# Kernel optimization log

Measured on AMD Instinct MI355X. Metric: run time of the kernel, lower is better.

## Reference

```python
import jax, jax.numpy as jnp
import numpy as np

N_NODES = 50000


def gcn_conv(x, src, dst, W, b, n_nodes):
    """PyG GCNConv: self-loops + symmetric normalization D^-1/2 (A+I) D^-1/2 X W + b."""
    loop = jnp.arange(n_nodes, dtype=src.dtype)
    s = jnp.concatenate([src, loop])
    d = jnp.concatenate([dst, loop])
    deg = jax.ops.segment_sum(jnp.ones_like(d, dtype=x.dtype), d, num_segments=n_nodes)
    dinv = jnp.where(deg > 0, jax.lax.rsqrt(deg), 0.0)
    norm = dinv[s] * dinv[d]  # (E+N,)
    h = x @ W  # (N, out)
    msg = h[s] * norm[:, None]
    return jax.ops.segment_sum(msg, d, num_segments=n_nodes) + b


def setup_inputs() -> dict:
    key = jax.random.key(0)
    ks = jax.random.split(key, 16)
    N, S, D = N_NODES, 20, 128
    E = 1_600_000
    PH, PO, GH, GO = 64, 128, 128, 32

    def lin(k, fan_in, fan_out):
        bound = 1.0 / np.sqrt(fan_in)
        kw, kb = jax.random.split(k)
        W = jax.random.uniform(kw, (fan_in, fan_out), jnp.float32, -bound, bound)
        b = jax.random.uniform(kb, (fan_out,), jnp.float32, -bound, bound)
        return W, b

    W_embed, b_embed = lin(ks[0], D, PH)
    W_attn, b_attn = lin(ks[1], PH, 1)
    W_out, b_out = lin(ks[2], PH, PO)
    W1, b1 = lin(ks[3], PO, GH)
    W2, b2 = lin(ks[4], GH, GO)
    Wm1, bm1 = lin(ks[5], GO, 64)
    Wm2, bm2 = lin(ks[6], 64, 1)

    return {
        "set_features": jax.random.normal(ks[7], (N, S, D), jnp.float32),
        "set_mask": jnp.ones((N, S), jnp.int32),
        "edge_index": jax.random.randint(ks[8], (2, E), 0, N, jnp.int32),
        "query_idx": jax.random.randint(ks[9], (4096,), 0, N, jnp.int32),
        "W_embed": W_embed, "b_embed": b_embed,
        "W_attn": W_attn, "b_attn": b_attn,
        "W_out": W_out, "b_out": b_out,
        "W1": W1, "b1": b1, "W2": W2, "b2": b2,
        "Wm1": Wm1, "bm1": bm1, "Wm2": Wm2, "bm2": bm2,
    }


def reference(set_features, set_mask, edge_index, query_idx,
              W_embed, b_embed, W_attn, b_attn, W_out, b_out,
              W1, b1, W2, b2, Wm1, bm1, Wm2, bm2):
    n_nodes = set_features.shape[0]
    # Attention pooling over each node's set: (N, S, D) -> (N, PO)
    z = jax.nn.relu(set_features @ W_embed + b_embed)          # (N, S, PH)
    scores = (z @ W_attn)[..., 0] + b_attn[0]                  # (N, S)
    scores = jnp.where(set_mask == 0, -jnp.inf, scores)
    attn = jax.nn.softmax(scores, axis=1)                      # (N, S)
    pooled = jnp.einsum('nsh,ns->nh', z, attn) @ W_out + b_out  # (N, PO)

    src, dst = edge_index[0], edge_index[1]
    x = jax.nn.relu(gcn_conv(pooled, src, dst, W1, b1, n_nodes))
    x = jax.nn.relu(gcn_conv(x, src, dst, W2, b2, n_nodes))

    q = x[query_idx]                                            # (B, GO)
    logits = (jax.nn.relu(q @ Wm1 + bm1) @ Wm2 + bm2)[..., 0]   # (B,)
    return logits
```

## Files before the change

kernel.cpp:

```cpp
#include <hip/hip_runtime.h>
#include <math.h>

#define RFL(x) __builtin_amdgcn_readfirstlane(x)
#define RL(x, l) __int_as_float(__builtin_amdgcn_readlane(__float_as_int(x), (l)))

typedef __attribute__((ext_vector_type(8))) short bf16x8;
typedef __attribute__((ext_vector_type(4))) float f32x4;

__device__ inline unsigned short bf16_rne(float f) {
  unsigned u = __float_as_uint(f);
  u += 0x7FFFu + ((u >> 16) & 1u);
  return (unsigned short)(u >> 16);
}


__global__ __launch_bounds__(256) void k_zero(int* p, int n) {
  int t = blockIdx.x * 256 + threadIdx.x;
  if (t < n) p[t] = 0;
}

__global__ __launch_bounds__(256) void k_count(const int* __restrict__ dst, int* cnt, int E) {
  int stride = gridDim.x * blockDim.x;
  for (int e = blockIdx.x * blockDim.x + threadIdx.x; e < E; e += stride)
    atomicAdd(&cnt[dst[e]], 1);
}


__global__ __launch_bounds__(256) void k_scan1(const int* __restrict__ cnt, int* __restrict__ row,
                                               int* __restrict__ partial, int N) {
  __shared__ int sm[256];
  int t = threadIdx.x, g = blockIdx.x * 256 + t;
  int v = (g < N) ? cnt[g] : 0;
  sm[t] = v;
  __syncthreads();
#pragma unroll
  for (int off = 1; off < 256; off <<= 1) {
    int x = 0;
    if (t >= off) x = sm[t - off];
    __syncthreads();
    if (t >= off) sm[t] += x;
    __syncthreads();
  }
  if (g < N) row[g] = sm[t] - v;
  if (t == 255) partial[blockIdx.x] = sm[255];
}

__global__ __launch_bounds__(256) void k_scan3(int* __restrict__ row, const int* __restrict__ partial,
                                               int* __restrict__ cursor, const int* __restrict__ cnt,
                                               float* __restrict__ dinv, int N) {
  __shared__ int red[256];
  const int t = threadIdx.x;
  int acc = 0;
  for (int i = t; i < blockIdx.x; i += 256) acc += partial[i];
  red[t] = acc;
  __syncthreads();
#pragma unroll
  for (int off = 128; off > 0; off >>= 1) {
    if (t < off) red[t] += red[t + off];
    __syncthreads();
  }
  const int base = red[0];
  int g = blockIdx.x * 256 + t;
  if (g < N) {
    int v = row[g] + base;
    row[g] = v;
    cursor[g] = v;
    dinv[g] = rsqrtf((float)cnt[g] + 1.0f);
  }
}


__global__ __launch_bounds__(256) void k_edge_fill(const int* __restrict__ src, const int* __restrict__ dst,
                                                   int* __restrict__ cursor, int* __restrict__ esrc, int E) {
  int stride = gridDim.x * blockDim.x;
  for (int e = blockIdx.x * blockDim.x + threadIdx.x; e < E; e += stride) {
    int s = src[e], d = dst[e];
    int pos = atomicAdd(&cursor[d], 1);
    esrc[pos] = s;
  }
}


__global__ __launch_bounds__(256) void k_wc(const float* __restrict__ Wout, const float* __restrict__ bout,
                                            const float* __restrict__ W1, float* __restrict__ Wc,
                                            float* __restrict__ bc) {
  int t = blockIdx.x * 256 + threadIdx.x;
  if (t >= 65 * 128) return;
  int h = t >> 7, o = t & 127;
  const float* row = (h < 64) ? (Wout + h * 128) : bout;
  float a = 0.f;
  for (int d = 0; d < 128; ++d) a += row[d] * W1[d * 128 + o];
  if (h < 64) Wc[h * 128 + o] = a;
  else bc[o] = a;
}


__global__ __launch_bounds__(256, 3) void k_pool(const float* __restrict__ X, const int* __restrict__ mask,
                                                 const float* __restrict__ WE, const float* __restrict__ bE,
                                                 const float* __restrict__ WA, const float* __restrict__ bA,
                                                 const float* __restrict__ dinv, float* __restrict__ pzp, int N) {
  __shared__ __align__(16) unsigned short Xh[80][136];
  __shared__ float scorep[80][4];
  __shared__ float sco[80];
  __shared__ float wgtA[80];
  float* zt = (float*)&Xh[0][0];

  const int t = threadIdx.x;
  const int lane = t & 63;
  const int wv = t >> 6;
  const int cb = wv * 16;
  const int l16 = lane & 15;
  const int lg = lane >> 4;

  const long long totRows = (long long)N * 20;
  const int numTiles = (N + 3) / 4;

  const int r0 = t >> 5;
  const int kq4 = (t & 31) * 4;

  bf16x8 bh[4], bl[4];
#pragma unroll
  for (int kk = 0; kk < 4; ++kk) {
    union { bf16x8 v; unsigned short s[8]; } uh, ul;
#pragma unroll
    for (int i = 0; i < 8; ++i) {
      int k = kk * 32 + lg * 8 + i;
      float w = WE[k * 64 + cb + l16];
      unsigned short h = bf16_rne(w);
      uh.s[i] = h;
      ul.s[i] = bf16_rne(w - __uint_as_float((unsigned)h << 16));
    }
    bh[kk] = uh.v;
    bl[kk] = ul.v;
  }
  const float bEv = bE[cb + l16];
  const float WAv = WA[cb + l16];
  const float bAv = bA[0];
  const float NEG = -3.0e38f;

  int tile = blockIdx.x;
  if (tile >= numTiles) return;

  float4 xv[10];
#pragma unroll
  for (int q = 0; q < 10; ++q) {
    long long rr = (long long)tile * 80 + r0 + q * 8;
    if (rr >= totRows) rr = totRows - 1;
    xv[q] = *(const float4*)(X + rr * 128 + kq4);
  }
  int mkcur = 1;
  {
    long long mi = (long long)tile * 80 + t;
    if (t < 80) mkcur = (mi < totRows) ? mask[mi] : 0;
  }

  while (true) {
#pragma unroll
    for (int q = 0; q < 10; ++q) {
      const int r = r0 + q * 8;
      const float4 v = xv[q];
      *(ushort4*)&Xh[r][kq4] = make_ushort4(bf16_rne(v.x), bf16_rne(v.y), bf16_rne(v.z), bf16_rne(v.w));
    }
    __syncthreads();

    const int nextTile = tile + gridDim.x;
    const bool hasNext = nextTile < numTiles;
    float4 xn[10];
    int mknext = 1;
    {
      const long long nb = (long long)(hasNext ? nextTile : tile) * 80;
#pragma unroll
      for (int q = 0; q < 10; ++q) {
        long long rr = nb + r0 + q * 8;
        if (rr >= totRows) rr = totRows - 1;
        xn[q] = *(const float4*)(X + rr * 128 + kq4);
      }
      long long mi = nb + t;
      if (t < 80) mknext = (mi < totRows) ? mask[mi] : 0;
    }

    f32x4 acc[5];
#pragma unroll
    for (int rt = 0; rt < 5; ++rt) acc[rt] = (f32x4){0.f, 0.f, 0.f, 0.f};
#pragma unroll
    for (int rt = 0; rt < 5; ++rt) {
      const int rl = rt * 16 + l16;
#pragma unroll
      for (int kk = 0; kk < 4; ++kk) {
        const int ko = kk * 32 + lg * 8;
        bf16x8 ah = *(const bf16x8*)&Xh[rl][ko];
        acc[rt] = __builtin_amdgcn_mfma_f32_16x16x32_bf16(ah, bh[kk], acc[rt], 0, 0, 0);
        acc[rt] = __builtin_amdgcn_mfma_f32_16x16x32_bf16(ah, bl[kk], acc[rt], 0, 0, 0);
      }
    }

#pragma unroll
    for (int rt = 0; rt < 5; ++rt) {
#pragma unroll
      for (int j = 0; j < 4; ++j) {
        float z = fmaxf(acc[rt][j] + bEv, 0.f);
        acc[rt][j] = z;
        float v = z * WAv;
        v += __shfl_xor(v, 1, 64);
        v += __shfl_xor(v, 2, 64);
        v += __shfl_xor(v, 4, 64);
        v += __shfl_xor(v, 8, 64);
        if (l16 == 0) scorep[rt * 16 + lg * 4 + j][wv] = v;
      }
    }
    __syncthreads();

#pragma unroll
    for (int rt = 0; rt < 5; ++rt) {
#pragma unroll
      for (int j = 0; j < 4; ++j) {
        int row = rt * 16 + lg * 4 + j;
        zt[row * 68 + cb + l16] = acc[rt][j];
      }
    }
    if (t < 80) {
      float4 sp = *(const float4*)scorep[t];
      float sc = sp.x + sp.y + sp.z + sp.w + bAv;
      if (mkcur == 0) sc = NEG;
      sco[t] = sc;
    }
    __syncthreads();

    if (t < 80) {
      const int base = (t / 20) * 20;
      float mx = NEG;
#pragma unroll
      for (int i = 0; i < 20; ++i) mx = fmaxf(mx, sco[base + i]);
      float den = 0.f;
#pragma unroll
      for (int i = 0; i < 20; ++i) den += __expf(sco[base + i] - mx);
      wgtA[t] = __expf(sco[t] - mx) / den;
    }
    __syncthreads();

    {
      int n = t >> 6, col = t & 63;
      long long node = (long long)tile * 4 + n;
      if (node < N) {
        float s = 0.f;
#pragma unroll
        for (int i = 0; i < 20; ++i) s += zt[(n * 20 + i) * 68 + col] * wgtA[n * 20 + i];
        pzp[node * 64 + col] = s * dinv[node];
      }
    }

    if (!hasNext) break;
    __syncthreads();
#pragma unroll
    for (int q = 0; q < 10; ++q) xv[q] = xn[q];
    mkcur = mknext;
    tile = nextTile;
  }
}


__global__ __launch_bounds__(256) void k_gather1(const int* __restrict__ row, const int* __restrict__ cnt,
                                                 const int* __restrict__ esrc, const float* __restrict__ pzp,
                                                 const float* __restrict__ dinv, float* __restrict__ y,
                                                 float* __restrict__ gout, int N) {
  const int lane = threadIdx.x & 63;
  const int node = RFL(blockIdx.x * 4 + (threadIdx.x >> 6));
  if (node >= N) return;
  const int q = lane >> 4, f4 = lane & 15;
  const int rs = RFL(row[node]);
  const int ne = RFL(cnt[node]);
  const float di = dinv[node];
  const float4* __restrict__ hv = (const float4*)pzp;
  float a0 = 0.f, a1 = 0.f, a2 = 0.f, a3 = 0.f, ds = 0.f;
  int j = 0;
  for (; j + 16 <= ne; j += 16) {
    const int b = rs + j + q * 4;
    int s[4];
#pragma unroll
    for (int u = 0; u < 4; ++u) s[u] = esrc[b + u];
    float4 v[4];
#pragma unroll
    for (int u = 0; u < 4; ++u) v[u] = hv[(size_t)s[u] * 16 + f4];
#pragma unroll
    for (int u = 0; u < 4; ++u) {
      a0 += v[u].x; a1 += v[u].y; a2 += v[u].z; a3 += v[u].w;
      ds += dinv[s[u]];
    }
  }
  if (j < ne) {
    const int b = j + q * 4;
    int s[4];
    float m[4];
#pragma unroll
    for (int u = 0; u < 4; ++u) {
      int idx = b + u;
      int c = (idx < ne) ? idx : (ne - 1);
      s[u] = esrc[rs + c];
      m[u] = (idx < ne) ? 1.f : 0.f;
    }
    float4 v[4];
#pragma unroll
    for (int u = 0; u < 4; ++u) v[u] = hv[(size_t)s[u] * 16 + f4];
#pragma unroll
    for (int u = 0; u < 4; ++u) {
      a0 += v[u].x * m[u]; a1 += v[u].y * m[u]; a2 += v[u].z * m[u]; a3 += v[u].w * m[u];
      ds += dinv[s[u]] * m[u];
    }
  }
  a0 += __shfl_xor(a0, 16, 64); a0 += __shfl_xor(a0, 32, 64);
  a1 += __shfl_xor(a1, 16, 64); a1 += __shfl_xor(a1, 32, 64);
  a2 += __shfl_xor(a2, 16, 64); a2 += __shfl_xor(a2, 32, 64);
  a3 += __shfl_xor(a3, 16, 64); a3 += __shfl_xor(a3, 32, 64);
  ds += __shfl_xor(ds, 16, 64); ds += __shfl_xor(ds, 32, 64);
  if (lane < 16) {
    float4 sv = hv[(size_t)node * 16 + f4];
    float4 o;
    o.x = (a0 + sv.x * di) * di;
    o.y = (a1 + sv.y * di) * di;
    o.z = (a2 + sv.z * di) * di;
    o.w = (a3 + sv.w * di) * di;
    ((float4*)y)[(size_t)node * 16 + f4] = o;
    if (f4 == 0) gout[node] = di * (ds + di * di);
  }
}


__global__ __launch_bounds__(256, 2) void k_gemm1(const float* __restrict__ y, const float* __restrict__ gin,
                                                  const float* __restrict__ Wc, const float* __restrict__ bc,
                                                  float* __restrict__ x1, int N) {
  const int lane = threadIdx.x & 63;
  float w0[64], w1[64];
#pragma unroll
  for (int d = 0; d < 64; ++d) {
    w0[d] = Wc[d * 128 + lane];
    w1[d] = Wc[d * 128 + 64 + lane];
  }
  const float b0 = bc[lane], b1v = bc[64 + lane];
  const int nw = (gridDim.x * blockDim.x) >> 6;
  const int w_id = (blockIdx.x * blockDim.x + threadIdx.x) >> 6;
  for (int r = w_id; r < N; r += nw) {
    const float xv = y[(size_t)r * 64 + lane];
    const float gr = gin[r];
    const int xi = __float_as_int(xv);
    float p0 = 0.f, p1 = 0.f, p2 = 0.f, p3 = 0.f;
#pragma unroll
    for (int d0 = 0; d0 < 64; d0 += 2) {
      float a0 = RL((float&)xi, d0);
      float a1 = RL((float&)xi, d0 + 1);
      p0 += a0 * w0[d0];
      p1 += a0 * w1[d0];
      p2 += a1 * w0[d0 + 1];
      p3 += a1 * w1[d0 + 1];
    }
    size_t o = (size_t)r * 128 + lane;
    x1[o] = p0 + p2 + gr * b0;
    x1[o + 64] = p1 + p3 + gr * b1v;
  }
}


__global__ __launch_bounds__(256, 2) void k_gemm2(const float* __restrict__ x1, const float* __restrict__ b1,
                                                  const float* __restrict__ W2, const float* __restrict__ dinv,
                                                  float* __restrict__ h2p, int N) {
  const int lane = threadIdx.x & 63;
  const int col = lane & 31;
  float w[128];
#pragma unroll
  for (int d = 0; d < 128; ++d) w[d] = W2[d * 32 + col];
  const float bb0 = b1[lane], bb1 = b1[64 + lane];
  const int nw = (gridDim.x * blockDim.x) >> 6;
  const int w_id = (blockIdx.x * blockDim.x + threadIdx.x) >> 6;
  for (int r = w_id; r < N; r += nw) {
    float rx0 = fmaxf(x1[(size_t)r * 128 + lane] + bb0, 0.f);
    float rx1 = fmaxf(x1[(size_t)r * 128 + 64 + lane] + bb1, 0.f);
    const int xi0 = __float_as_int(rx0), xi1 = __float_as_int(rx1);
    float p0 = 0.f, p1 = 0.f, p2 = 0.f, p3 = 0.f;
#pragma unroll
    for (int d0 = 0; d0 < 64; d0 += 2) {
      float a0 = RL((float&)xi0, d0);
      float a1 = RL((float&)xi0, d0 + 1);
      float c0 = RL((float&)xi1, d0);
      float c1 = RL((float&)xi1, d0 + 1);
      p0 += a0 * w[d0];
      p1 += a1 * w[d0 + 1];
      p2 += c0 * w[64 + d0];
      p3 += c1 * w[64 + d0 + 1];
    }
    if (lane < 32) {
      float di = dinv[r];
      h2p[(size_t)r * 32 + col] = ((p0 + p1) + (p2 + p3)) * di;
    }
  }
}


__global__ __launch_bounds__(256) void k_gmlp(const int* __restrict__ qidx, const int* __restrict__ row,
                                              const int* __restrict__ cnt, const int* __restrict__ esrc,
                                              const float* __restrict__ h2p, const float* __restrict__ dinv,
                                              const float* __restrict__ b2, const float* __restrict__ Wm1,
                                              const float* __restrict__ bm1, const float* __restrict__ Wm2,
                                              const float* __restrict__ bm2, float* __restrict__ out, int B) {
  __shared__ float qs[4][32];
  const int lane = threadIdx.x & 63;
  const int wv = threadIdx.x >> 6;
  const int w = blockIdx.x * 4 + wv;
  const int wc = (w < B) ? w : (B - 1);
  const int node = RFL(qidx[wc]);

  const int q = lane >> 3, f4 = lane & 7;
  const int rs = RFL(row[node]);
  const int ne = RFL(cnt[node]);
  const float di = dinv[node];
  const float4* __restrict__ hv = (const float4*)h2p;
  float a0 = 0.f, a1 = 0.f, a2 = 0.f, a3 = 0.f;
  int j = 0;
  for (; j + 32 <= ne; j += 32) {
    const int b = rs + j + q * 4;
    int s[4];
#pragma unroll
    for (int u = 0; u < 4; ++u) s[u] = esrc[b + u];
    float4 v[4];
#pragma unroll
    for (int u = 0; u < 4; ++u) v[u] = hv[(size_t)s[u] * 8 + f4];
#pragma unroll
    for (int u = 0; u < 4; ++u) {
      a0 += v[u].x; a1 += v[u].y; a2 += v[u].z; a3 += v[u].w;
    }
  }
  if (j < ne) {
    const int b = j + q * 4;
    int s[4];
    float m[4];
#pragma unroll
    for (int u = 0; u < 4; ++u) {
      int idx = b + u;
      int c = (idx < ne) ? idx : (ne - 1);
      s[u] = esrc[rs + c];
      m[u] = (idx < ne) ? 1.f : 0.f;
    }
    float4 v[4];
#pragma unroll
    for (int u = 0; u < 4; ++u) v[u] = hv[(size_t)s[u] * 8 + f4];
#pragma unroll
    for (int u = 0; u < 4; ++u) {
      a0 += v[u].x * m[u]; a1 += v[u].y * m[u]; a2 += v[u].z * m[u]; a3 += v[u].w * m[u];
    }
  }
#pragma unroll
  for (int off = 8; off <= 32; off <<= 1) {
    a0 += __shfl_xor(a0, off, 64);
    a1 += __shfl_xor(a1, off, 64);
    a2 += __shfl_xor(a2, off, 64);
    a3 += __shfl_xor(a3, off, 64);
  }
  if (q == 0) {
    float4 sv = hv[(size_t)node * 8 + f4];
    qs[wv][f4 * 4 + 0] = fmaxf((a0 + sv.x * di) * di + b2[f4 * 4 + 0], 0.f);
    qs[wv][f4 * 4 + 1] = fmaxf((a1 + sv.y * di) * di + b2[f4 * 4 + 1], 0.f);
    qs[wv][f4 * 4 + 2] = fmaxf((a2 + sv.z * di) * di + b2[f4 * 4 + 2], 0.f);
    qs[wv][f4 * 4 + 3] = fmaxf((a3 + sv.w * di) * di + b2[f4 * 4 + 3], 0.f);
  }
  __syncthreads();

  float h = bm1[lane];
#pragma unroll
  for (int k = 0; k < 32; ++k) h += qs[wv][k] * Wm1[k * 64 + lane];
  float r = fmaxf(h, 0.f) * Wm2[lane];
#pragma unroll
  for (int off = 1; off < 64; off <<= 1) r += __shfl_xor(r, off, 64);
  if (lane == 0 && w < B) out[w] = r + bm2[0];
}


extern "C" void kernel_launch(void* const* d_in, const int* in_sizes, int n_in,
                              void* d_out, int out_size, void* d_ws, size_t ws_size,
                              hipStream_t stream) {
  const float* X    = (const float*)d_in[0];
  const int*   mask = (const int*)d_in[1];
  const int*   ei   = (const int*)d_in[2];
  const int*   qidx = (const int*)d_in[3];
  const float* WE   = (const float*)d_in[4];
  const float* bE   = (const float*)d_in[5];
  const float* WA   = (const float*)d_in[6];
  const float* bA   = (const float*)d_in[7];
  const float* Wout = (const float*)d_in[8];
  const float* bout = (const float*)d_in[9];
  const float* W1   = (const float*)d_in[10];
  const float* b1   = (const float*)d_in[11];
  const float* W2   = (const float*)d_in[12];
  const float* b2   = (const float*)d_in[13];
  const float* Wm1  = (const float*)d_in[14];
  const float* bm1  = (const float*)d_in[15];
  const float* Wm2  = (const float*)d_in[16];
  const float* bm2  = (const float*)d_in[17];

  const int N = in_sizes[1] / 20;
  const int E = in_sizes[2] / 2;
  const int B = in_sizes[3];
  const int* src  = ei;
  const int* dstp = ei + E;

  const size_t Na = ((size_t)N + 63) & ~(size_t)63;
  const size_t Ea = ((size_t)E + 63) & ~(size_t)63;
  const int P = (N + 255) / 256;
  const size_t Pa = ((size_t)P + 63) & ~(size_t)63;

  float* ws      = (float*)d_ws;
  float* dinv    = ws;
  int*   cnt     = (int*)(dinv + Na);
  int*   rowp    = cnt + Na;
  int*   cursor  = rowp + Na;
  int*   partial = cursor + Na;
  int*   esrc    = partial + Pa;
  float* Wc      = (float*)(esrc + Ea);
  float* bc      = Wc + 8192;
  float* gbuf    = bc + 128;
  float* pzp     = gbuf + Na;
  float* y       = pzp + (size_t)N * 64;
  float* x1      = y + (size_t)N * 64;
  float* h2p     = pzp;

  const int nb = (N + 255) / 256;
  const int nw4 = (N + 3) / 4;
  const int poolBlocks = ((N + 3) / 4 < 768) ? (N + 3) / 4 : 768;

  k_zero<<<nb, 256, 0, stream>>>(cnt, N);
  k_count<<<1024, 256, 0, stream>>>(dstp, cnt, E);
  k_scan1<<<P, 256, 0, stream>>>(cnt, rowp, partial, N);
  k_scan3<<<P, 256, 0, stream>>>(rowp, partial, cursor, cnt, dinv, N);
  k_edge_fill<<<2048, 256, 0, stream>>>(src, dstp, cursor, esrc, E);
  k_wc<<<33, 256, 0, stream>>>(Wout, bout, W1, Wc, bc);
  k_pool<<<poolBlocks, 256, 0, stream>>>(X, mask, WE, bE, WA, bA, dinv, pzp, N);
  k_gather1<<<nw4, 256, 0, stream>>>(rowp, cnt, esrc, pzp, dinv, y, gbuf, N);
  k_gemm1<<<1024, 256, 0, stream>>>(y, gbuf, Wc, bc, x1, N);
  k_gemm2<<<1024, 256, 0, stream>>>(x1, b1, W2, dinv, h2p, N);
  k_gmlp<<<(B + 3) / 4, 256, 0, stream>>>(qidx, rowp, cnt, esrc, h2p, dinv, b2, Wm1, bm1, Wm2, bm2,
                                          (float*)d_out, B);
}
```

Measured before the change: 460.1 us.

## Double-buffer LDS tiles in k_pool to prefetch two tiles ahead

The pooling kernel now keeps two bf16 LDS tile buffers. It writes the next tile into the alternate buffer during the current tile's epilogue and issues global loads two tiles ahead, removing one barrier-separated staging phase per iteration. The aim is to hide global load latency behind the MFMA and softmax work. In exchange, LDS use roughly doubles, which may lower occupancy under the 3-blocks-per-SM launch bound, and register pressure rises a little.

```diff
diff --git a/kernel.cpp b/kernel.cpp
--- a/kernel.cpp
+++ b/kernel.cpp
@@ -99,11 +99,11 @@
                                                  const float* __restrict__ WE, const float* __restrict__ bE,
                                                  const float* __restrict__ WA, const float* __restrict__ bA,
                                                  const float* __restrict__ dinv, float* __restrict__ pzp, int N) {
-  __shared__ __align__(16) unsigned short Xh[80][136];
+  __shared__ __align__(16) unsigned short XA[80][136];
+  __shared__ __align__(16) unsigned short XB[80][136];
   __shared__ float scorep[80][4];
   __shared__ float sco[80];
   __shared__ float wgtA[80];
-  float* zt = (float*)&Xh[0][0];
 
   const int t = threadIdx.x;
   const int lane = t & 63;
@@ -153,31 +153,32 @@
     long long mi = (long long)tile * 80 + t;
     if (t < 80) mkcur = (mi < totRows) ? mask[mi] : 0;
   }
-
+#pragma unroll
+  for (int q = 0; q < 10; ++q) {
+    const float4 v = xv[q];
+    *(ushort4*)&XA[r0 + q * 8][kq4] = make_ushort4(bf16_rne(v.x), bf16_rne(v.y), bf16_rne(v.z), bf16_rne(v.w));
+  }
+  int nextTile = tile + gridDim.x;
+  bool hasNext = nextTile < numTiles;
+  int mknext = 1;
+  {
+    const long long nb = (long long)(hasNext ? nextTile : tile) * 80;
+#pragma unroll
+    for (int q = 0; q < 10; ++q) {
+      long long rr = nb + r0 + q * 8;
+      if (rr >= totRows) rr = totRows - 1;
+      xv[q] = *(const float4*)(X + rr * 128 + kq4);
+    }
+    long long mi = nb + t;
+    if (t < 80) mknext = (mi < totRows) ? mask[mi] : 0;
+  }
+  __syncthreads();
+
+  int cur = 0;
   while (true) {
-#pragma unroll
-    for (int q = 0; q < 10; ++q) {
-      const int r = r0 + q * 8;
-      const float4 v = xv[q];
-      *(ushort4*)&Xh[r][kq4] = make_ushort4(bf16_rne(v.x), bf16_rne(v.y), bf16_rne(v.z), bf16_rne(v.w));
-    }
-    __syncthreads();
-
-    const int nextTile = tile + gridDim.x;
-    const bool hasNext = nextTile < numTiles;
-    float4 xn[10];
-    int mknext = 1;
-    {
-      const long long nb = (long long)(hasNext ? nextTile : tile) * 80;
-#pragma unroll
-      for (int q = 0; q < 10; ++q) {
-        long long rr = nb + r0 + q * 8;
-        if (rr >= totRows) rr = totRows - 1;
-        xn[q] = *(const float4*)(X + rr * 128 + kq4);
-      }
-      long long mi = nb + t;
-      if (t < 80) mknext = (mi < totRows) ? mask[mi] : 0;
-    }
+    unsigned short(*curB)[136] = cur ? XB : XA;
+    unsigned short(*othB)[136] = cur ? XA : XB;
+    float* zt = (float*)&curB[0][0];
 
     f32x4 acc[5];
 #pragma unroll
@@ -188,7 +189,7 @@
 #pragma unroll
       for (int kk = 0; kk < 4; ++kk) {
         const int ko = kk * 32 + lg * 8;
-        bf16x8 ah = *(const bf16x8*)&Xh[rl][ko];
+        bf16x8 ah = *(const bf16x8*)&curB[rl][ko];
         acc[rt] = __builtin_amdgcn_mfma_f32_16x16x32_bf16(ah, bh[kk], acc[rt], 0, 0, 0);
         acc[rt] = __builtin_amdgcn_mfma_f32_16x16x32_bf16(ah, bl[kk], acc[rt], 0, 0, 0);
       }
@@ -208,6 +209,26 @@
         if (l16 == 0) scorep[rt * 16 + lg * 4 + j][wv] = v;
       }
     }
+
+#pragma unroll
+    for (int q = 0; q < 10; ++q) {
+      const float4 v = xv[q];
+      *(ushort4*)&othB[r0 + q * 8][kq4] = make_ushort4(bf16_rne(v.x), bf16_rne(v.y), bf16_rne(v.z), bf16_rne(v.w));
+    }
+    const int tile2 = nextTile + gridDim.x;
+    const bool has2 = tile2 < numTiles;
+    int mk2 = 1;
+    {
+      const long long nb = (long long)(has2 ? tile2 : tile) * 80;
+#pragma unroll
+      for (int q = 0; q < 10; ++q) {
+        long long rr = nb + r0 + q * 8;
+        if (rr >= totRows) rr = totRows - 1;
+        xv[q] = *(const float4*)(X + rr * 128 + kq4);
+      }
+      long long mi = nb + t;
+      if (t < 80) mk2 = (mi < totRows) ? mask[mi] : 0;
+    }
     __syncthreads();
 
 #pragma unroll
@@ -251,10 +272,12 @@
 
     if (!hasNext) break;
     __syncthreads();
-#pragma unroll
-    for (int q = 0; q < 10; ++q) xv[q] = xn[q];
+    tile = nextTile;
+    nextTile = tile2;
+    hasNext = has2;
     mkcur = mknext;
-    tile = nextTile;
+    mknext = mk2;
+    cur ^= 1;
   }
 }
 
```

Measured after the change: 479.9 us. +4.3%, slower.
